# Optimization experiments

Measured on AMD Instinct MI355X. Metric: run time of the kernel, lower is better.

The kernel has to match this reference:

```python
import jax, jax.numpy as jnp
import numpy as np

B, T, H, K = 64, 1024, 256, 4  # batch, seq_len, hidden_dim, crf_size


def setup_inputs() -> dict:
    key = jax.random.key(0)
    ks = jax.random.split(key, 8)
    return {
        "sentence_features": jax.random.normal(ks[0], (B, T, H), dtype=jnp.float32),
        "conv_w": jax.random.normal(ks[1], (H, H, 3), dtype=jnp.float32) * (1.0 / np.sqrt(3 * H)),
        "conv_b": jnp.zeros((H,), dtype=jnp.float32),
        "lin_w": jax.random.normal(ks[2], (K, H), dtype=jnp.float32) * (1.0 / np.sqrt(H)),
        "lin_b": jnp.zeros((K,), dtype=jnp.float32),
        "crf_start": jax.random.uniform(ks[3], (K,), dtype=jnp.float32, minval=-0.1, maxval=0.1),
        "crf_end": jax.random.uniform(ks[4], (K,), dtype=jnp.float32, minval=-0.1, maxval=0.1),
        "crf_trans": jax.random.uniform(ks[5], (K, K), dtype=jnp.float32, minval=-0.1, maxval=0.1),
    }


def _emissions(x, conv_w, conv_b, lin_w, lin_b):
    # x: [B, T, H] -> transpose -> Conv1d(k=3, pad=1) -> ReLU -> transpose -> Linear
    xc = jnp.swapaxes(x, 1, 2)  # [B, H, T]
    y = jax.lax.conv_general_dilated(
        xc, conv_w, window_strides=(1,), padding=((1, 1),),
        dimension_numbers=("NCH", "OIH", "NCH"))
    y = jax.nn.relu(y + conv_b[None, :, None])
    y = jnp.swapaxes(y, 1, 2)  # [B, T, H]
    return y @ lin_w.T + lin_b  # [B, T, K]


def _viterbi_decode(em, start, end, trans):
    # em: [B, T, K]; torchcrf CRF.decode with no mask (batch_first=True)
    score0 = start[None, :] + em[:, 0]  # [B, K]

    def step(score, emit_t):
        # score [B, K] over prev tag; broadcast to [B, K_prev, K_next]
        nxt = score[:, :, None] + trans[None, :, :] + emit_t[:, None, :]
        return jnp.max(nxt, axis=1), jnp.argmax(nxt, axis=1)  # new score, best prev tag

    em_rest = jnp.swapaxes(em[:, 1:], 0, 1)  # [T-1, B, K]
    final, history = jax.lax.scan(step, score0, em_rest)
    final = final + end[None, :]
    last_tag = jnp.argmax(final, axis=-1)  # [B]

    def back(tag, idx_t):
        prev = jnp.take_along_axis(idx_t, tag[:, None], axis=1)[:, 0]
        return prev, prev

    _, tags_head = jax.lax.scan(back, last_tag, history, reverse=True)  # [T-1, B]
    path = jnp.concatenate([jnp.swapaxes(tags_head, 0, 1), last_tag[:, None]], axis=1)
    return path.astype(jnp.int32)  # [B, T]


def reference(sentence_features, conv_w, conv_b, lin_w, lin_b, crf_start, crf_end, crf_trans):
    em = _emissions(sentence_features, conv_w, conv_b, lin_w, lin_b)
    return _viterbi_decode(em, crf_start, crf_end, crf_trans)
```

## Files before the change

kernel.cpp:

```cpp
#include <hip/hip_runtime.h>
#include <cstdint>
#include <cstddef>

typedef __attribute__((ext_vector_type(8))) short short8;
typedef __attribute__((ext_vector_type(4))) float f32x4;

constexpr int Bn = 64, Tn = 1024, Hn = 256, Kn = 4;
constexpr int TT = 64;
constexpr int AROWS = TT + 2;
constexpr int ARSTR = 144;
constexpr int ABUFSZ = AROWS * ARSTR;

__device__ __forceinline__ unsigned bf16rne(float f) {
  unsigned u = __float_as_uint(f);
  return (u + 0x7fffu + ((u >> 16) & 1u)) >> 16;
}

__global__ __launch_bounds__(256) void pack_b_k(const float* __restrict__ conv_w,
                                                unsigned short* __restrict__ Bp) {
  int gt = blockIdx.x * 256 + threadIdx.x;
  int fid = gt >> 6, l = gt & 63;
  int ks = fid >> 5, rem = fid & 31;
  int p = rem >> 4, nf = rem & 15;
  int n = nf * 16 + (l & 15);
  int k0 = ks * 32 + ((l >> 4) << 3);
  short8 s;
  #pragma unroll
  for (int j = 0; j < 8; ++j) {
    int k = k0 + j;
    int dt = k >> 8, i = k & 255;
    float w = conv_w[n * 768 + i * 3 + dt];
    unsigned hb = bf16rne(w);
    if (p == 0) s[j] = (short)hb;
    else        s[j] = (short)bf16rne(w - __uint_as_float(hb << 16));
  }
  *reinterpret_cast<short8*>(Bp + (size_t)fid * 512 + l * 8) = s;
}

#define GBAR() asm volatile("s_waitcnt lgkmcnt(0)\n\ts_barrier" ::: "memory")

__global__ __launch_bounds__(256, 2) void emis_k(const float* __restrict__ x,
    const unsigned short* __restrict__ Bp, const float* __restrict__ conv_b,
    const float* __restrict__ lin_w, float* __restrict__ em2) {
  __shared__ __align__(16) char A_lds[2 * ABUFSZ];

  const int b = blockIdx.z, ny = blockIdx.y, t0 = blockIdx.x * TT;
  const int tid = threadIdx.x, lane = tid & 63, w = tid >> 6;
  const int wm = w >> 1, wn = w & 1;
  const float* xb = x + (size_t)b * Tn * Hn;

  float4 pre[3];

  auto loadA = [&](int ig) {
    #pragma unroll
    for (int it = 0; it < 3; ++it) {
      int idx = it * 256 + tid;
      if (idx < AROWS * 8) {
        int row = idx >> 3, c4 = idx & 7;
        int trow = t0 - 1 + row;
        float4 v = make_float4(0.f, 0.f, 0.f, 0.f);
        if (trow >= 0 && trow < Tn)
          v = *reinterpret_cast<const float4*>(xb + (size_t)trow * Hn + ig * 32 + c4 * 4);
        pre[it] = v;
      }
    }
  };
  auto writeA = [&](int boff) {
    #pragma unroll
    for (int it = 0; it < 3; ++it) {
      int idx = it * 256 + tid;
      if (idx < AROWS * 8) {
        int row = idx >> 3, c4 = idx & 7;
        float vf[4] = {pre[it].x, pre[it].y, pre[it].z, pre[it].w};
        unsigned h[4], lo[4];
        #pragma unroll
        for (int q = 0; q < 4; ++q) {
          h[q] = bf16rne(vf[q]);
          lo[q] = bf16rne(vf[q] - __uint_as_float(h[q] << 16));
        }
        uint2 hp, lp;
        hp.x = h[0] | (h[1] << 16);  hp.y = h[2] | (h[3] << 16);
        lp.x = lo[0] | (lo[1] << 16); lp.y = lo[2] | (lo[3] << 16);
        char* base = A_lds + boff + row * ARSTR + c4 * 8;
        *reinterpret_cast<uint2*>(base) = hp;
        *reinterpret_cast<uint2*>(base + 64) = lp;
      }
    }
  };

  const char* bsrc = reinterpret_cast<const char*>(Bp)
      + (size_t)(ny * 8 + wn * 4) * 1024 + lane * 16;
  auto loadB = [&](short8* Bh, short8* Bl, int ks) {
    #pragma unroll
    for (int nf = 0; nf < 4; ++nf) {
      Bh[nf] = *reinterpret_cast<const short8*>(bsrc + (size_t)((ks * 2 + 0) * 16 + nf) * 1024);
      Bl[nf] = *reinterpret_cast<const short8*>(bsrc + (size_t)((ks * 2 + 1) * 16 + nf) * 1024);
    }
  };

  f32x4 acc[2][4];
  #pragma unroll
  for (int mf = 0; mf < 2; ++mf)
    #pragma unroll
    for (int nf = 0; nf < 4; ++nf) acc[mf][nf] = (f32x4)0.f;

  const char* aB = A_lds + (lane & 15) * ARSTR + ((lane >> 4) << 4) + wm * 32 * ARSTR;

  short8 BhA[4], BlA[4], BhB[4], BlB[4];

#define STEP(ABUF, DT, BH, BL, NBH, NBL, KSN)                                 \
  {                                                                           \
    loadB(NBH, NBL, (KSN));                                                   \
    __builtin_amdgcn_s_setprio(1);                                            \
    _Pragma("unroll")                                                         \
    for (int mf = 0; mf < 2; ++mf) {                                          \
      const char* ap = aB + (ABUF) + (mf * 16 + (DT)) * ARSTR;                \
      short8 Ah = *reinterpret_cast<const short8*>(ap);                       \
      short8 Al = *reinterpret_cast<const short8*>(ap + 64);                  \
      _Pragma("unroll")                                                       \
      for (int nf = 0; nf < 4; ++nf) {                                        \
        f32x4 c = acc[mf][nf];                                                \
        c = __builtin_amdgcn_mfma_f32_16x16x32_bf16(Ah, BH[nf], c, 0, 0, 0);  \
        c = __builtin_amdgcn_mfma_f32_16x16x32_bf16(Al, BH[nf], c, 0, 0, 0);  \
        c = __builtin_amdgcn_mfma_f32_16x16x32_bf16(Ah, BL[nf], c, 0, 0, 0);  \
        acc[mf][nf] = c;                                                      \
      }                                                                       \
    }                                                                         \
    __builtin_amdgcn_s_setprio(0);                                            \
  }

  loadA(0);
  loadB(BhA, BlA, 0);
  writeA(0);
  GBAR();

  #pragma unroll 1
  for (int igp = 0; igp < 4; ++igp) {
    const int ig0 = igp * 2, ig1 = ig0 + 1;
    loadA(ig1);
    STEP(0, 0, BhA, BlA, BhB, BlB, 8 + ig0);
    STEP(0, 1, BhB, BlB, BhA, BlA, 16 + ig0);
    STEP(0, 2, BhA, BlA, BhB, BlB, ig1);
    writeA(ABUFSZ);
    GBAR();
    if (ig1 < 7) loadA(ig1 + 1);
    STEP(ABUFSZ, 0, BhB, BlB, BhA, BlA, 8 + ig1);
    STEP(ABUFSZ, 1, BhA, BlA, BhB, BlB, 16 + ig1);
    STEP(ABUFSZ, 2, BhB, BlB, BhA, BlA, (ig1 < 7 ? ig1 + 1 : 0));
    if (ig1 < 7) writeA(0);
    GBAR();
  }
#undef STEP

  f32x4 pem[2][4];
  #pragma unroll
  for (int mf = 0; mf < 2; ++mf)
    #pragma unroll
    for (int v = 0; v < 4; ++v) pem[mf][v] = (f32x4)0.f;

  #pragma unroll
  for (int nf = 0; nf < 4; ++nf) {
    const int gcol = ny * 128 + wn * 64 + nf * 16 + (lane & 15);
    const float cb = conv_b[gcol];
    f32x4 lw;
    lw[0] = lin_w[gcol]; lw[1] = lin_w[256 + gcol];
    lw[2] = lin_w[512 + gcol]; lw[3] = lin_w[768 + gcol];
    #pragma unroll
    for (int mf = 0; mf < 2; ++mf)
      #pragma unroll
      for (int v = 0; v < 4; ++v) {
        float val = fmaxf(acc[mf][nf][v] + cb, 0.f);
        pem[mf][v] += val * lw;
      }
  }
  #pragma unroll
  for (int mf = 0; mf < 2; ++mf)
    #pragma unroll
    for (int v = 0; v < 4; ++v) {
      f32x4 t = pem[mf][v];
      #pragma unroll
      for (int m = 1; m < 16; m <<= 1) {
        f32x4 q;
        q[0] = __shfl_xor(t[0], m); q[1] = __shfl_xor(t[1], m);
        q[2] = __shfl_xor(t[2], m); q[3] = __shfl_xor(t[3], m);
        t += q;
      }
      pem[mf][v] = t;
    }
  __syncthreads();
  float* red = reinterpret_cast<float*>(A_lds);
  if ((lane & 15) == 0) {
    const int g = lane >> 4;
    #pragma unroll
    for (int mf = 0; mf < 2; ++mf)
      #pragma unroll
      for (int v = 0; v < 4; ++v) {
        int r = wm * 32 + mf * 16 + g * 4 + v;
        *reinterpret_cast<f32x4*>(red + (r * 2 + wn) * 4) = pem[mf][v];
      }
  }
  __syncthreads();
  if (tid < TT) {
    f32x4 s0 = *reinterpret_cast<f32x4*>(red + tid * 8);
    f32x4 s1 = *reinterpret_cast<f32x4*>(red + tid * 8 + 4);
    f32x4 s = s0 + s1;
    *reinterpret_cast<f32x4*>(em2 + ((size_t)(b * Tn + t0 + tid) * 2 + ny) * 4) = s;
  }
}

__device__ __forceinline__ unsigned int compose_map(unsigned int a, unsigned int b) {
#if __has_builtin(__builtin_amdgcn_perm)
  return __builtin_amdgcn_perm(a, a, b);
#else
  unsigned int c = 0;
  #pragma unroll
  for (int k = 0; k < 4; ++k) {
    unsigned int sel = (b >> (8 * k)) & 0xffu;
    c |= ((a >> (8 * sel)) & 0xffu) << (8 * k);
  }
  return c;
#endif
}

template <int J>
__device__ __forceinline__ float qb(float v) {
  return __int_as_float(__builtin_amdgcn_update_dpp(
      0, __float_as_int(v), (J * 0x55), 0xf, 0xf, true));
}

#define PSTEP(EV, T)                                                       \
  {                                                                        \
    shf[((T) - 1) * 4 + kk] = s;                                           \
    float c0 = qb<0>(s) + trc0;                                            \
    float c1 = qb<1>(s) + trc1;                                            \
    float c2 = qb<2>(s) + trc2;                                            \
    float c3 = qb<3>(s) + trc3;                                            \
    s = fmaxf(fmaxf(c0, c1), fmaxf(c2, c3)) + (EV);                        \
  }

__global__ __launch_bounds__(64) void viterbi_k(const float* __restrict__ em2,
    const float* __restrict__ lin_b, const float* __restrict__ cstart,
    const float* __restrict__ cend, const float* __restrict__ ctrans,
    int* __restrict__ out) {
  __shared__ float4 se[Tn];
  __shared__ float4 sh[Tn - 1];
  __shared__ int s_last;
  const int b = blockIdx.x, lane = threadIdx.x;
  const float4* e2 = reinterpret_cast<const float4*>(em2 + (size_t)b * Tn * 8);
  const float lb0 = lin_b[0], lb1 = lin_b[1], lb2 = lin_b[2], lb3 = lin_b[3];
  for (int i = lane; i < Tn; i += 64) {
    float4 a = e2[i * 2], c = e2[i * 2 + 1];
    se[i] = make_float4(a.x + c.x + lb0, a.y + c.y + lb1,
                        a.z + c.z + lb2, a.w + c.w + lb3);
  }
  float tr[4][4];
  #pragma unroll
  for (int j = 0; j < 4; ++j)
    #pragma unroll
    for (int k = 0; k < 4; ++k) tr[j][k] = ctrans[j * 4 + k];
  __syncthreads();

  if (lane < 4) {
    const int kk = lane;
    const float* sef = reinterpret_cast<const float*>(se);
    float* shf = reinterpret_cast<float*>(sh);
    const float trc0 = ctrans[0 * 4 + kk];
    const float trc1 = ctrans[1 * 4 + kk];
    const float trc2 = ctrans[2 * 4 + kk];
    const float trc3 = ctrans[3 * 4 + kk];
    float s = cstart[kk] + sef[kk];
    float e[8];
    #pragma unroll
    for (int d = 0; d < 8; ++d) e[d] = sef[(1 + d) * 4 + kk];
    int t = 1;
    #pragma unroll 1
    for (int g = 0; g < 127; ++g, t += 8) {
      float f[8];
      #pragma unroll
      for (int d = 0; d < 8; ++d) f[d] = e[d];
      #pragma unroll
      for (int d = 0; d < 8; ++d) e[d] = sef[(t + 8 + d) * 4 + kk];
      PSTEP(f[0], t);     PSTEP(f[1], t + 1);
      PSTEP(f[2], t + 2); PSTEP(f[3], t + 3);
      PSTEP(f[4], t + 4); PSTEP(f[5], t + 5);
      PSTEP(f[6], t + 6); PSTEP(f[7], t + 7);
    }
    PSTEP(e[0], 1017); PSTEP(e[1], 1018); PSTEP(e[2], 1019);
    PSTEP(e[3], 1020); PSTEP(e[4], 1021); PSTEP(e[5], 1022);
    PSTEP(e[6], 1023);
    s += cend[kk];
    float f0 = __shfl(s, 0), f1 = __shfl(s, 1);
    float f2 = __shfl(s, 2), f3 = __shfl(s, 3);
    if (kk == 0) {
      int tag = 0; float bf = f0;
      if (f1 > bf) { bf = f1; tag = 1; }
      if (f2 > bf) { bf = f2; tag = 2; }
      if (f3 > bf) { bf = f3; tag = 3; }
      s_last = tag;
    }
  }
  __syncthreads();

  const unsigned int ID = 0x03020100u;
  unsigned int mloc[16];
  const int t0 = lane * 16;
  #pragma unroll
  for (int k = 0; k < 16; ++k) {
    const int t = t0 + k;
    if (t < Tn - 1) {
      const float4 s = sh[t];
      const float4 e = se[t + 1];
      const float sj[4] = {s.x, s.y, s.z, s.w};
      const float ev[4] = {e.x, e.y, e.z, e.w};
      unsigned int mw = 0;
      #pragma unroll
      for (int kk = 0; kk < 4; ++kk) {
        float best = (sj[0] + tr[0][kk]) + ev[kk];
        int bi = 0;
        #pragma unroll
        for (int j = 1; j < 4; ++j) {
          float cc = (sj[j] + tr[j][kk]) + ev[kk];
          if (cc > best) { best = cc; bi = j; }
        }
        mw |= (unsigned)bi << (8 * kk);
      }
      mloc[k] = mw;
    } else {
      mloc[k] = ID;
    }
  }
  unsigned int P = mloc[15];
  #pragma unroll
  for (int k = 14; k >= 0; --k) P = compose_map(mloc[k], P);
  #pragma unroll
  for (int d = 1; d < 64; d <<= 1) {
    unsigned int q = (unsigned int)__shfl_down((int)P, d);
    if (lane + d > 63) q = ID;
    P = compose_map(P, q);
  }
  unsigned int E = (unsigned int)__shfl_down((int)P, 1);
  if (lane == 63) E = ID;
  const int last = s_last;
  unsigned int tag = (E >> (8 * last)) & 3u;
  int* ob = out + (size_t)b * Tn;
  #pragma unroll
  for (int k = 15; k >= 0; --k) {
    tag = (mloc[k] >> (8 * tag)) & 3u;
    ob[t0 + k] = (int)tag;
  }
}

extern "C" void kernel_launch(void* const* d_in, const int* in_sizes, int n_in,
                              void* d_out, int out_size, void* d_ws, size_t ws_size,
                              hipStream_t stream) {
  const float* x      = (const float*)d_in[0];
  const float* conv_w = (const float*)d_in[1];
  const float* conv_b = (const float*)d_in[2];
  const float* lin_w  = (const float*)d_in[3];
  const float* lin_b  = (const float*)d_in[4];
  const float* cstart = (const float*)d_in[5];
  const float* cend   = (const float*)d_in[6];
  const float* ctrans = (const float*)d_in[7];
  int* out = (int*)d_out;

  unsigned short* Bp = (unsigned short*)d_ws;
  float* em2 = (float*)((char*)d_ws + 786432);

  pack_b_k<<<192, 256, 0, stream>>>(conv_w, Bp);
  emis_k<<<dim3(Tn / TT, 2, Bn), 256, 0, stream>>>(x, Bp, conv_b, lin_w, em2);
  viterbi_k<<<Bn, 64, 0, stream>>>(em2, lin_b, cstart, cend, ctrans, out);
}
```

Baseline: 123.7 us.

## Give each wave a private LDS A-tile and drop block barriers

Each wave now stages its own 34-row halo slice of the input tile into a private double-buffered LDS region instead of sharing a 66-row block tile. This removes every workgroup barrier from the main loop, so waves no longer wait on one another. In exchange the two waves that share a row range load and convert the same A data twice, raising global loads and LDS usage. Correctness within a wave relies on in-order LDS access without explicit waits.

```diff
diff --git a/kernel.cpp b/kernel.cpp
--- a/kernel.cpp
+++ b/kernel.cpp
@@ -7,9 +7,9 @@
 
 constexpr int Bn = 64, Tn = 1024, Hn = 256, Kn = 4;
 constexpr int TT = 64;
-constexpr int AROWS = TT + 2;
+constexpr int WROWS = 34;
 constexpr int ARSTR = 144;
-constexpr int ABUFSZ = AROWS * ARSTR;
+constexpr int WBUF = WROWS * ARSTR;
 
 __device__ __forceinline__ unsigned bf16rne(float f) {
   unsigned u = __float_as_uint(f);
@@ -37,27 +37,26 @@
   *reinterpret_cast<short8*>(Bp + (size_t)fid * 512 + l * 8) = s;
 }
 
-#define GBAR() asm volatile("s_waitcnt lgkmcnt(0)\n\ts_barrier" ::: "memory")
-
 __global__ __launch_bounds__(256, 2) void emis_k(const float* __restrict__ x,
     const unsigned short* __restrict__ Bp, const float* __restrict__ conv_b,
     const float* __restrict__ lin_w, float* __restrict__ em2) {
-  __shared__ __align__(16) char A_lds[2 * ABUFSZ];
+  __shared__ __align__(16) char A_lds[4 * 2 * WBUF];
 
   const int b = blockIdx.z, ny = blockIdx.y, t0 = blockIdx.x * TT;
   const int tid = threadIdx.x, lane = tid & 63, w = tid >> 6;
   const int wm = w >> 1, wn = w & 1;
   const float* xb = x + (size_t)b * Tn * Hn;
-
-  float4 pre[3];
+  char* const wlds = A_lds + w * (2 * WBUF);
+
+  float4 pre[5];
 
   auto loadA = [&](int ig) {
     #pragma unroll
-    for (int it = 0; it < 3; ++it) {
-      int idx = it * 256 + tid;
-      if (idx < AROWS * 8) {
+    for (int it = 0; it < 5; ++it) {
+      int idx = it * 64 + lane;
+      if (idx < WROWS * 8) {
         int row = idx >> 3, c4 = idx & 7;
-        int trow = t0 - 1 + row;
+        int trow = t0 + wm * 32 - 1 + row;
         float4 v = make_float4(0.f, 0.f, 0.f, 0.f);
         if (trow >= 0 && trow < Tn)
           v = *reinterpret_cast<const float4*>(xb + (size_t)trow * Hn + ig * 32 + c4 * 4);
@@ -67,9 +66,9 @@
   };
   auto writeA = [&](int boff) {
     #pragma unroll
-    for (int it = 0; it < 3; ++it) {
-      int idx = it * 256 + tid;
-      if (idx < AROWS * 8) {
+    for (int it = 0; it < 5; ++it) {
+      int idx = it * 64 + lane;
+      if (idx < WROWS * 8) {
         int row = idx >> 3, c4 = idx & 7;
         float vf[4] = {pre[it].x, pre[it].y, pre[it].z, pre[it].w};
         unsigned h[4], lo[4];
@@ -81,7 +80,7 @@
         uint2 hp, lp;
         hp.x = h[0] | (h[1] << 16);  hp.y = h[2] | (h[3] << 16);
         lp.x = lo[0] | (lo[1] << 16); lp.y = lo[2] | (lo[3] << 16);
-        char* base = A_lds + boff + row * ARSTR + c4 * 8;
+        char* base = wlds + boff + row * ARSTR + c4 * 8;
         *reinterpret_cast<uint2*>(base) = hp;
         *reinterpret_cast<uint2*>(base + 64) = lp;
       }
@@ -104,7 +103,7 @@
     #pragma unroll
     for (int nf = 0; nf < 4; ++nf) acc[mf][nf] = (f32x4)0.f;
 
-  const char* aB = A_lds + (lane & 15) * ARSTR + ((lane >> 4) << 4) + wm * 32 * ARSTR;
+  const char* aB = wlds + (lane & 15) * ARSTR + ((lane >> 4) << 4);
 
   short8 BhA[4], BlA[4], BhB[4], BlB[4];
 
@@ -132,7 +131,6 @@
   loadA(0);
   loadB(BhA, BlA, 0);
   writeA(0);
-  GBAR();
 
   #pragma unroll 1
   for (int igp = 0; igp < 4; ++igp) {
@@ -141,14 +139,12 @@
     STEP(0, 0, BhA, BlA, BhB, BlB, 8 + ig0);
     STEP(0, 1, BhB, BlB, BhA, BlA, 16 + ig0);
     STEP(0, 2, BhA, BlA, BhB, BlB, ig1);
-    writeA(ABUFSZ);
-    GBAR();
+    writeA(WBUF);
     if (ig1 < 7) loadA(ig1 + 1);
-    STEP(ABUFSZ, 0, BhB, BlB, BhA, BlA, 8 + ig1);
-    STEP(ABUFSZ, 1, BhA, BlA, BhB, BlB, 16 + ig1);
-    STEP(ABUFSZ, 2, BhB, BlB, BhA, BlA, (ig1 < 7 ? ig1 + 1 : 0));
+    STEP(WBUF, 0, BhB, BlB, BhA, BlA, 8 + ig1);
+    STEP(WBUF, 1, BhA, BlA, BhB, BlB, 16 + ig1);
+    STEP(WBUF, 2, BhB, BlB, BhA, BlA, (ig1 < 7 ? ig1 + 1 : 0));
     if (ig1 < 7) writeA(0);
-    GBAR();
   }
 #undef STEP
 
```

After: 158.2 us. 1.28x slower.
